# Optimization experiments

Hardware: AMD Instinct MI355X
Metric: run time of the kernel (lower is better)

The kernel has to match this reference:

```python
import jax, jax.numpy as jnp
import numpy as np
from jax import lax

# Covers the fully-specified prefix of ColorHead.downgrade (the high-headroom region):
# ColorDownsample(16) -> ModePool2d(11,1,1) -> Conv1x1(3->32) -> depthwise Conv1x1 -> BN -> LeakyReLU
#   -> Conv1x1(32->32) -> depthwise Conv1x1 -> BN -> LeakyReLU

NBINS = 17
KS = 11  # ModePool2d kernel_size
EPS = 1e-5
SLOPE = 0.01  # torch LeakyReLU default negative_slope


def color_downsample(x, down=16.0):
    return jnp.round(x * 255.0 / down) * down / 256.0


def mode_pool2d(x, kernel_size=KS, stride=1, padding=1):
    # Equivalent to torch unfold + scatter_add histogram + argmax, but computes
    # per-bin counts with a windowed sum over one-hot indicators (no giant unfold).
    xp = jnp.pad(x, ((0, 0), (0, 0), (padding, padding), (padding, padding)))
    bins = jnp.clip(jnp.round(xp * 16.0), 0.0, 16.0).astype(jnp.int32)  # [B,C,H,W]
    onehot = (bins[:, :, None, :, :] == jnp.arange(NBINS, dtype=jnp.int32)[None, None, :, None, None]).astype(x.dtype)  # [B,C,17,H,W]
    counts = lax.reduce_window(
        onehot, jnp.array(0, x.dtype), lax.add,
        window_dimensions=(1, 1, 1, kernel_size, kernel_size),
        window_strides=(1, 1, 1, stride, stride),
        padding='VALID')  # [B,C,17,Ho,Wo]
    mode_bins = jnp.argmax(counts, axis=2)  # first max, like torch argmax
    return mode_bins.astype(x.dtype) / 16.0


def conv1x1(x, w, b):
    # w: [O, C], b: [O]
    return jnp.einsum('bchw,oc->bohw', x, w) + b[None, :, None, None]


def dwconv1x1(x, w, b):
    # depthwise 1x1 (groups == channels): per-channel affine. w: [C], b: [C]
    return x * w[None, :, None, None] + b[None, :, None, None]


def batchnorm(x, gamma, beta):
    # training-mode BN: batch statistics over (B,H,W)
    mean = jnp.mean(x, axis=(0, 2, 3), keepdims=True)
    var = jnp.var(x, axis=(0, 2, 3), keepdims=True)
    xn = (x - mean) * lax.rsqrt(var + EPS)
    return xn * gamma[None, :, None, None] + beta[None, :, None, None]


def leaky_relu(x):
    return jnp.where(x >= 0, x, SLOPE * x)


def setup_inputs() -> dict:
    key = jax.random.key(0)
    ks = jax.random.split(key, 8)
    C_in, C_h = 3, 32
    x = jax.random.uniform(ks[0], (8, C_in, 512, 512), dtype=jnp.float32)
    w1 = jax.random.normal(ks[1], (C_h, C_in), dtype=jnp.float32) * 0.1
    b1 = jnp.zeros((C_h,), jnp.float32)
    wd1 = jax.random.normal(ks[2], (C_h,), dtype=jnp.float32) * 0.1 + 1.0
    bd1 = jnp.zeros((C_h,), jnp.float32)
    g1 = jnp.ones((C_h,), jnp.float32)
    be1 = jnp.zeros((C_h,), jnp.float32)
    w2 = jax.random.normal(ks[3], (C_h, C_h), dtype=jnp.float32) * 0.1
    b2 = jnp.zeros((C_h,), jnp.float32)
    wd2 = jax.random.normal(ks[4], (C_h,), dtype=jnp.float32) * 0.1 + 1.0
    bd2 = jnp.zeros((C_h,), jnp.float32)
    g2 = jnp.ones((C_h,), jnp.float32)
    be2 = jnp.zeros((C_h,), jnp.float32)
    return dict(x=x, w1=w1, b1=b1, wd1=wd1, bd1=bd1, g1=g1, be1=be1,
                w2=w2, b2=b2, wd2=wd2, bd2=bd2, g2=g2, be2=be2)


def reference(x, w1, b1, wd1, bd1, g1, be1, w2, b2, wd2, bd2, g2, be2):
    h = color_downsample(x)
    h = mode_pool2d(h)                      # [B,3,504,504]
    h = conv1x1(h, w1, b1)                  # [B,32,504,504]
    h = dwconv1x1(h, wd1, bd1)
    h = leaky_relu(batchnorm(h, g1, be1))
    h = conv1x1(h, w2, b2)
    h = dwconv1x1(h, wd2, bd2)
    h = leaky_relu(batchnorm(h, g2, be2))
    return h
```

## Files before the change

### kernel.cpp

```cpp
#include <hip/hip_runtime.h>
#include <hip/hip_bf16.h>

typedef unsigned char u8;
typedef unsigned short u16;
typedef unsigned int u32;

#define PP     254016
#define PADW   514
#define PADP   264196
#define NPIX   2032128
#define NTRIP  4913
#define N_F    2032128.0
#define RROWS  14

__device__ __forceinline__ float bf2f(__hip_bfloat16 h){ return __bfloat162float(h); }
__device__ __forceinline__ u32 f2bf(float f){
  u32 u = __float_as_uint(f);
  return ((u + 0x7FFFu + ((u >> 16) & 1u)) >> 16);
}
__device__ __forceinline__ float ldv(const void* p, int i, u32 f){
  return f ? ((const float*)p)[i] : bf2f(((const __hip_bfloat16*)p)[i]);
}

__global__ __launch_bounds__(256) void k_init(const u16* __restrict__ xw, u32* __restrict__ flag,
                                              u32* __restrict__ hist){
  int t = threadIdx.x;
  for (int i=t; i<NTRIP; i+=256) hist[i] = 0u;
  if (t < 64){
    u32 bad = 0;
    for (int i=t; i<1024; i+=64) bad |= (u32)(xw[i] >> 15);
    int anybad = __any((int)bad);
    if (t == 0) *flag = anybad ? 1u : 0u;
  }
}

__global__ __launch_bounds__(256) void k_bins(const void* __restrict__ x, u8* __restrict__ bins,
                                              const u32* __restrict__ flag){
  u32 f = *flag;
  int plane = blockIdx.y;
  int pix = blockIdx.x*256 + threadIdx.x;
  if (pix >= PADP) return;
  int r = pix / PADW; int c = pix - r*PADW;
  u8 v = 0;
  if (r >= 1 && r <= 512 && c >= 1 && c <= 512){
    float xv = ldv(x, plane*262144 + (r-1)*512 + (c-1), f);
    v = (u8)(int)rintf((xv * 255.0f) * 0.0625f);
  }
  bins[(size_t)plane*PADP + pix] = v;
}

__global__ __launch_bounds__(512) void k_mode(const u8* __restrict__ bins, u8* __restrict__ modes){
  int plane = blockIdx.y;
  int r0 = blockIdx.x * RROWS;
  const u8* bp = bins + (size_t)plane*PADP;
  u8* mp = modes + (size_t)plane*PP;
  __shared__ u32 A0[2][516], A1[2][516];
  int t = threadIdx.x;
  bool extra = (t < 2);
  u32 v0=0, v1=0, w0=0, w1=0;
  #pragma unroll 1
  for (int j=0; j<11; j++){
    int row = r0 + j;
    { int b = bp[row*PADW + t]; u32 d = 1u << ((b & 7)*4);
      v0 += (b < 8) ? d : 0u; v1 += (b >= 8 && b < 16) ? d : 0u; }
    if (extra){ int b = bp[row*PADW + 512 + t]; u32 d = 1u << ((b & 7)*4);
      w0 += (b < 8) ? d : 0u; w1 += (b >= 8 && b < 16) ? d : 0u; }
  }
  A0[0][t] = v0; A1[0][t] = v1;
  if (extra){ A0[0][512+t] = w0; A1[0][512+t] = w1; }
  __syncthreads();
  for (int i=0; i<RROWS; i++){
    int r = r0 + i;
    int cur = i & 1, nxt = cur ^ 1;
    if (t < 504){
      u32 h0=0,h1=0,h2=0,h3=0;
      #pragma unroll
      for (int dx=0; dx<11; dx++){
        u32 n0 = A0[cur][t+dx], n1 = A1[cur][t+dx];
        h0 += n0 & 0x0F0F0F0Fu;
        h1 += (n0 >> 4) & 0x0F0F0F0Fu;
        h2 += n1 & 0x0F0F0F0Fu;
        h3 += (n1 >> 4) & 0x0F0F0F0Fu;
      }
      u32 T = h0 + h1 + h2 + h3;
      u32 s = (T & 0xFFu) + ((T>>8)&0xFFu) + ((T>>16)&0xFFu) + (T>>24);
      u32 best = (121u - s) << 5;
      #pragma unroll
      for (int b=0;b<16;b++){
        u32 word = (b & 1) ? ((b < 8) ? h1 : h3) : ((b < 8) ? h0 : h2);
        u32 cnt = (word >> (((b >> 1) & 3) * 8)) & 0xFFu;
        u32 key = (cnt << 5) | (u32)(16 - b);
        best = (key > best) ? key : best;
      }
      mp[r*504 + t] = (u8)(16u - (best & 31u));
    }
    if (i+1 < RROWS){
      { int b = bp[r*PADW + t]; u32 d = 1u << ((b & 7)*4);
        v0 -= (b < 8) ? d : 0u; v1 -= (b >= 8 && b < 16) ? d : 0u; }
      { int b = bp[(r+11)*PADW + t]; u32 d = 1u << ((b & 7)*4);
        v0 += (b < 8) ? d : 0u; v1 += (b >= 8 && b < 16) ? d : 0u; }
      if (extra){
        { int b = bp[r*PADW + 512 + t]; u32 d = 1u << ((b & 7)*4);
          w0 -= (b < 8) ? d : 0u; w1 -= (b >= 8 && b < 16) ? d : 0u; }
        { int b = bp[(r+11)*PADW + 512 + t]; u32 d = 1u << ((b & 7)*4);
          w0 += (b < 8) ? d : 0u; w1 += (b >= 8 && b < 16) ? d : 0u; }
      }
      A0[nxt][t] = v0; A1[nxt][t] = v1;
      if (extra){ A0[nxt][512+t] = w0; A1[nxt][512+t] = w1; }
    }
    __syncthreads();
  }
}

__global__ __launch_bounds__(256) void k_triple(const u8* __restrict__ modes, u16* __restrict__ triple, u32* __restrict__ hist){
  __shared__ u32 lh[NTRIP];
  for (int i=threadIdx.x;i<NTRIP;i+=256) lh[i]=0;
  __syncthreads();
  int stride = gridDim.x*256;
  for (int p = blockIdx.x*256 + threadIdx.x; p < NPIX; p += stride){
    int bimg = p / PP; int pix = p - bimg*PP;
    const u8* mb = modes + (size_t)bimg*3*PP + pix;
    int m0 = mb[0], m1 = mb[PP], m2 = mb[2*PP];
    int idx = (m0*17 + m1)*17 + m2;
    triple[p] = (u16)idx;
    atomicAdd(&lh[idx], 1u);
  }
  __syncthreads();
  for (int i=threadIdx.x;i<NTRIP;i+=256){ u32 v = lh[i]; if (v) atomicAdd(&hist[i], v); }
}

__device__ __forceinline__ void compute_P1(const u32* __restrict__ hist,
    const void* w1, const void* b1, const void* wd1, const void* bd1,
    const void* g1, const void* be1, u32 f, float* sP ,
    u32* wred , u32* mom ){
  u32 a0=0,a1=0,a2=0,a3=0,a4=0,a5=0,a6=0,a7=0,a8=0;
  for (int t=threadIdx.x; t<NTRIP; t+=256){
    u32 c = hist[t];
    int m2 = t % 17; int tt = t/17; int m1 = tt % 17; int m0 = tt/17;
    a0 += c*m0; a1 += c*m1; a2 += c*m2;
    a3 += c*m0*m0; a4 += c*m1*m1; a5 += c*m2*m2;
    a6 += c*m0*m1; a7 += c*m0*m2; a8 += c*m1*m2;
  }
  #pragma unroll
  for (int s=1; s<64; s<<=1){
    a0 += __shfl_xor(a0,s); a1 += __shfl_xor(a1,s); a2 += __shfl_xor(a2,s);
    a3 += __shfl_xor(a3,s); a4 += __shfl_xor(a4,s); a5 += __shfl_xor(a5,s);
    a6 += __shfl_xor(a6,s); a7 += __shfl_xor(a7,s); a8 += __shfl_xor(a8,s);
  }
  int wv = threadIdx.x >> 6;
  if ((threadIdx.x & 63) == 0){
    wred[wv*9+0]=a0; wred[wv*9+1]=a1; wred[wv*9+2]=a2; wred[wv*9+3]=a3; wred[wv*9+4]=a4;
    wred[wv*9+5]=a5; wred[wv*9+6]=a6; wred[wv*9+7]=a7; wred[wv*9+8]=a8;
  }
  __syncthreads();
  if (threadIdx.x < 9) mom[threadIdx.x] = wred[threadIdx.x] + wred[9+threadIdx.x] + wred[18+threadIdx.x] + wred[27+threadIdx.x];
  __syncthreads();
  if (threadIdx.x < 32){
    int o = threadIdx.x;
    double wd = ldv(wd1,o,f);
    double q0 = wd*ldv(w1,o*3+0,f), q1 = wd*ldv(w1,o*3+1,f), q2 = wd*ldv(w1,o*3+2,f);
    double qc = wd*ldv(b1,o,f) + ldv(bd1,o,f);
    double S0=mom[0],S1=mom[1],S2=mom[2],S00=mom[3],S11=mom[4],S22=mom[5],S01=mom[6],S02=mom[7],S12=mom[8];
    double lin = (q0*S0 + q1*S1 + q2*S2) * (1.0/16.0);
    double mean = lin/N_F + qc;
    double quad = (q0*q0*S00 + q1*q1*S11 + q2*q2*S22 + 2.0*(q0*q1*S01 + q0*q2*S02 + q1*q2*S12)) * (1.0/256.0);
    double Ev2 = quad/N_F + 2.0*qc*lin/N_F + qc*qc;
    double var = Ev2 - mean*mean;
    double rstd = 1.0 / sqrt(var + 1e-5);
    double A = rstd * ldv(g1,o,f);
    double B = ldv(be1,o,f) - mean*A;
    sP[o]      = (float)(q0*A);
    sP[32+o]   = (float)(q1*A);
    sP[64+o]   = (float)(q2*A);
    sP[96+o]   = (float)(qc*A + B);
  }
  __syncthreads();
}

__global__ __launch_bounds__(256) void k_stats2(const u32* __restrict__ hist,
    const void* w1, const void* b1, const void* wd1, const void* bd1, const void* g1, const void* be1,
    const void* w2, const void* b2, const void* wd2, const void* bd2,
    double* __restrict__ sums2, const u32* __restrict__ flag){
  u32 f = *flag;
  int o = blockIdx.x;
  __shared__ float sP[128];
  __shared__ u32 wred[36], mom[9];
  __shared__ float sw[32];
  compute_P1(hist, w1,b1,wd1,bd1,g1,be1, f, sP, wred, mom);
  for (int i=threadIdx.x;i<32;i+=256) sw[i] = ldv(w2, o*32+i, f);
  __syncthreads();
  float wd = ldv(wd2, o, f);
  float cc = wd * ldv(b2, o, f) + ldv(bd2, o, f);
  double s=0.0, q=0.0;
  for (int t=threadIdx.x; t<NTRIP; t+=256){
    int m2 = t % 17; int tt = t / 17; int m1 = tt % 17; int m0 = tt / 17;
    float f0 = m0*(1.f/16.f), f1 = m1*(1.f/16.f), f2 = m2*(1.f/16.f);
    float dot = 0.f;
    #pragma unroll
    for (int c=0;c<32;c++){
      float u = sP[c]*f0 + sP[32+c]*f1 + sP[64+c]*f2 + sP[96+c];
      float y = (u >= 0.f) ? u : 0.01f*u;
      dot += sw[c]*y;
    }
    float v2 = wd*dot + cc;
    double cn = (double)hist[t];
    s += cn*(double)v2;
    q += cn*(double)v2*(double)v2;
  }
  __shared__ double red[256];
  red[threadIdx.x]=s; __syncthreads();
  for (int off=128; off>0; off>>=1){ if (threadIdx.x<off) red[threadIdx.x]+=red[threadIdx.x+off]; __syncthreads(); }
  if (threadIdx.x==0) sums2[o]=red[0];
  __syncthreads();
  red[threadIdx.x]=q; __syncthreads();
  for (int off=128; off>0; off>>=1){ if (threadIdx.x<off) red[threadIdx.x]+=red[threadIdx.x+off]; __syncthreads(); }
  if (threadIdx.x==0) sums2[32+o]=red[0];
}

__global__ __launch_bounds__(256) void k_lut(const u32* __restrict__ hist, const double* __restrict__ sums2,
    const void* w1, const void* b1, const void* wd1, const void* bd1, const void* g1, const void* be1,
    const void* w2, const void* b2, const void* wd2, const void* bd2,
    const void* g2, const void* be2,
    float* __restrict__ lutf, u32* __restrict__ lutb, const u32* __restrict__ flag){
  u32 f = *flag;
  __shared__ float sP[128];
  __shared__ u32 wred[36], mom[9];
  __shared__ float sw[1024];
  __shared__ float ka[32], kb[32];
  compute_P1(hist, w1,b1,wd1,bd1,g1,be1, f, sP, wred, mom);
  for (int i=threadIdx.x;i<1024;i+=256) sw[i]=ldv(w2, i, f);
  if (threadIdx.x < 32){
    int o = threadIdx.x;
    double mean = sums2[o] / N_F;
    double var  = sums2[32+o] / N_F - mean*mean;
    double rstd = 1.0 / sqrt(var + 1e-5);
    double A = rstd * (double)ldv(g2, o, f);
    double B = (double)ldv(be2, o, f) - mean*A;
    double wd = (double)ldv(wd2, o, f);
    ka[o] = (float)(wd*A);
    kb[o] = (float)((wd*(double)ldv(b2, o, f) + (double)ldv(bd2, o, f))*A + B);
  }
  __syncthreads();
  int t = blockIdx.x*256 + threadIdx.x;
  if (t >= NTRIP) return;
  int m2 = t % 17; int tt = t/17; int m1 = tt % 17; int m0 = tt/17;
  float f0=m0*(1.f/16.f), f1=m1*(1.f/16.f), f2=m2*(1.f/16.f);
  float y1[32];
  #pragma unroll
  for (int c=0;c<32;c++){
    float u = sP[c]*f0 + sP[32+c]*f1 + sP[64+c]*f2 + sP[96+c];
    y1[c] = (u>=0.f)?u:0.01f*u;
  }
  float y2[32];
  #pragma unroll
  for (int o=0;o<32;o++){
    float dot=0.f;
    #pragma unroll
    for (int c=0;c<32;c++) dot += sw[o*32+c]*y1[c];
    float v = dot*ka[o] + kb[o];
    y2[o] = (v>=0.f)?v:0.01f*v;
    lutf[t*32+o] = y2[o];
  }
  #pragma unroll
  for (int j=0;j<16;j++)
    lutb[t*16+j] = f2bf(y2[2*j]) | (f2bf(y2[2*j+1]) << 16);
}

__global__ __launch_bounds__(256) void k_out(const u16* __restrict__ triple, const float* __restrict__ lutf,
                                             const u32* __restrict__ lutb,
                                             void* __restrict__ out, const u32* __restrict__ flag){
  u32 f = *flag;
  int g = blockIdx.x*256 + threadIdx.x;
  if (g >= NPIX/2) return;
  int p0 = g*2;
  int bimg = p0 / PP; int pix = p0 - bimg*PP;
  u32 tt = *(const u32*)(triple + p0);
  u32 ia = tt & 0xFFFFu, ib = tt >> 16;
  if (f){
    const float4* La = (const float4*)(lutf + (size_t)ia*32);
    const float4* Lb = (const float4*)(lutf + (size_t)ib*32);
    float* ob = (float*)out + (size_t)bimg*32*PP + pix;
    #pragma unroll
    for (int j=0;j<8;j++){
      float4 a = La[j]; float4 b = Lb[j];
      float2 v;
      v.x=a.x; v.y=b.x; *(float2*)(ob + (size_t)(4*j+0)*PP) = v;
      v.x=a.y; v.y=b.y; *(float2*)(ob + (size_t)(4*j+1)*PP) = v;
      v.x=a.z; v.y=b.z; *(float2*)(ob + (size_t)(4*j+2)*PP) = v;
      v.x=a.w; v.y=b.w; *(float2*)(ob + (size_t)(4*j+3)*PP) = v;
    }
  } else {
    const uint4* La = (const uint4*)(lutb + (size_t)ia*16);
    const uint4* Lb = (const uint4*)(lutb + (size_t)ib*16);
    u16* ob = (u16*)out + (size_t)bimg*32*PP + pix;
    #pragma unroll
    for (int j=0;j<4;j++){
      uint4 A = La[j]; uint4 B = Lb[j];
      *(u32*)(ob + (size_t)(8*j+0)*PP) = __builtin_amdgcn_perm(B.x, A.x, 0x05040100u);
      *(u32*)(ob + (size_t)(8*j+1)*PP) = __builtin_amdgcn_perm(B.x, A.x, 0x07060302u);
      *(u32*)(ob + (size_t)(8*j+2)*PP) = __builtin_amdgcn_perm(B.y, A.y, 0x05040100u);
      *(u32*)(ob + (size_t)(8*j+3)*PP) = __builtin_amdgcn_perm(B.y, A.y, 0x07060302u);
      *(u32*)(ob + (size_t)(8*j+4)*PP) = __builtin_amdgcn_perm(B.z, A.z, 0x05040100u);
      *(u32*)(ob + (size_t)(8*j+5)*PP) = __builtin_amdgcn_perm(B.z, A.z, 0x07060302u);
      *(u32*)(ob + (size_t)(8*j+6)*PP) = __builtin_amdgcn_perm(B.w, A.w, 0x05040100u);
      *(u32*)(ob + (size_t)(8*j+7)*PP) = __builtin_amdgcn_perm(B.w, A.w, 0x07060302u);
    }
  }
}

extern "C" void kernel_launch(void* const* d_in, const int* in_sizes, int n_in,
                              void* d_out, int out_size, void* d_ws, size_t ws_size,
                              hipStream_t stream){
  const void* x   = d_in[0];
  const void* w1  = d_in[1];
  const void* b1  = d_in[2];
  const void* wd1 = d_in[3];
  const void* bd1 = d_in[4];
  const void* g1  = d_in[5];
  const void* be1 = d_in[6];
  const void* w2  = d_in[7];
  const void* b2  = d_in[8];
  const void* wd2 = d_in[9];
  const void* bd2 = d_in[10];
  const void* g2  = d_in[11];
  const void* be2 = d_in[12];

  char* w = (char*)d_ws;
  auto alloc = [&](size_t bytes)->char* { char* p = w; w += (bytes + 255) & ~(size_t)255; return p; };
  u32*   flag   = (u32*)  alloc(256);
  u8*    bins   = (u8*)   alloc(24ull*PADP);
  u8*    modes  = (u8*)   alloc(24ull*PP);
  u16*   triple = (u16*)  alloc(2ull*NPIX);
  u32*   hist   = (u32*)  alloc(4ull*NTRIP);
  double* sums2 = (double*)alloc(64ull*8);
  float* lutf   = (float*)alloc(4ull*NTRIP*32);
  u32*   lutb   = (u32*)  alloc(4ull*NTRIP*16);

  k_init<<<dim3(1), 256, 0, stream>>>((const u16*)x, flag, hist);
  k_bins<<<dim3((PADP+255)/256, 24), 256, 0, stream>>>(x, bins, flag);
  k_mode<<<dim3(36, 24), 512, 0, stream>>>(bins, modes);
  k_triple<<<dim3(1984), 256, 0, stream>>>(modes, triple, hist);
  k_stats2<<<dim3(32), 256, 0, stream>>>(hist, w1,b1,wd1,bd1,g1,be1, w2,b2,wd2,bd2, sums2, flag);
  k_lut<<<dim3((NTRIP+255)/256), 256, 0, stream>>>(hist, sums2, w1,b1,wd1,bd1,g1,be1,
                                                   w2,b2,wd2,bd2, g2,be2, lutf, lutb, flag);
  k_out<<<dim3((NPIX/2)/256), 256, 0, stream>>>(triple, lutf, lutb, d_out, flag);
}
```

Measured before the change: 442.6 us.

## Fuse binning, mode pooling and triple histogram into one kernel

Replaces the separate bin, mode-pool and triple/histogram kernels with a single kernel that reads the input directly, keeps all three channels' sliding column counts in 64-bit packed registers, and emits the triple index plus a shared-memory histogram. The intermediate bins and modes buffers and their global round trips go away, and the argmax uses packed 16-bit max operations. In exchange it reloads an input row for each slide step, uses a shorter row strip per block (4 rows, so more redundant 11-row warmup reads), and puts more shared-memory atomics in each block.

```diff
diff --git a/kernel.cpp b/kernel.cpp
--- a/kernel.cpp
+++ b/kernel.cpp
@@ -4,14 +4,14 @@
 typedef unsigned char u8;
 typedef unsigned short u16;
 typedef unsigned int u32;
+typedef unsigned long long u64;
 
 #define PP     254016
-#define PADW   514
-#define PADP   264196
 #define NPIX   2032128
 #define NTRIP  4913
 #define N_F    2032128.0
-#define RROWS  14
+#define RROWS  4
+#define NRB    126
 
 __device__ __forceinline__ float bf2f(__hip_bfloat16 h){ return __bfloat162float(h); }
 __device__ __forceinline__ u32 f2bf(float f){
@@ -21,6 +21,23 @@
 __device__ __forceinline__ float ldv(const void* p, int i, u32 f){
   return f ? ((const float*)p)[i] : bf2f(((const __hip_bfloat16*)p)[i]);
 }
+
+typedef unsigned short us2 __attribute__((ext_vector_type(2)));
+__device__ __forceinline__ u32 pkmax(u32 a, u32 b){
+  us2 x = __builtin_bit_cast(us2, a);
+  us2 y = __builtin_bit_cast(us2, b);
+  us2 r = __builtin_elementwise_max(x, y);
+  return __builtin_bit_cast(u32, r);
+}
+
+__device__ __forceinline__ u32 getbin(const void* x, u32 f, int img, int ch, int pr, int pc){
+  if ((u32)(pr-1) < 512u && (u32)(pc-1) < 512u){
+    float xv = ldv(x, ((img*3+ch)*512 + (pr-1))*512 + (pc-1), f);
+    return (u32)(int)rintf(xv * 255.0f * 0.0625f);
+  }
+  return 0u;
+}
+__device__ __forceinline__ u64 bdelta(u32 b){ return (b < 16u) ? (1ull << (b*4)) : 0ull; }
 
 __global__ __launch_bounds__(256) void k_init(const u16* __restrict__ xw, u32* __restrict__ flag,
                                               u32* __restrict__ hist){
@@ -34,99 +51,116 @@
   }
 }
 
-__global__ __launch_bounds__(256) void k_bins(const void* __restrict__ x, u8* __restrict__ bins,
-                                              const u32* __restrict__ flag){
+__global__ __launch_bounds__(512) void k_fused(const void* __restrict__ x, const u32* __restrict__ flag,
+                                               u16* __restrict__ triple, u32* __restrict__ hist){
   u32 f = *flag;
-  int plane = blockIdx.y;
-  int pix = blockIdx.x*256 + threadIdx.x;
-  if (pix >= PADP) return;
-  int r = pix / PADW; int c = pix - r*PADW;
-  u8 v = 0;
-  if (r >= 1 && r <= 512 && c >= 1 && c <= 512){
-    float xv = ldv(x, plane*262144 + (r-1)*512 + (c-1), f);
-    v = (u8)(int)rintf((xv * 255.0f) * 0.0625f);
-  }
-  bins[(size_t)plane*PADP + pix] = v;
-}
-
-__global__ __launch_bounds__(512) void k_mode(const u8* __restrict__ bins, u8* __restrict__ modes){
-  int plane = blockIdx.y;
+  int img = blockIdx.y;
   int r0 = blockIdx.x * RROWS;
-  const u8* bp = bins + (size_t)plane*PADP;
-  u8* mp = modes + (size_t)plane*PP;
-  __shared__ u32 A0[2][516], A1[2][516];
   int t = threadIdx.x;
+  __shared__ u64 CNT[3][518];
+  __shared__ u32 lh[NTRIP];
+  for (int i=t; i<NTRIP; i+=512) lh[i] = 0u;
+
   bool extra = (t < 2);
-  u32 v0=0, v1=0, w0=0, w1=0;
-  #pragma unroll 1
+  int colB = 512 + t;
+  u64 v[3] = {0,0,0}, vb[3] = {0,0,0};
+  u64 rn[3] = {0,0,0}, rnb[3] = {0,0,0};
+  u32 r16[3] = {0,0,0}, r16b[3] = {0,0,0};
+
   for (int j=0; j<11; j++){
-    int row = r0 + j;
-    { int b = bp[row*PADW + t]; u32 d = 1u << ((b & 7)*4);
-      v0 += (b < 8) ? d : 0u; v1 += (b >= 8 && b < 16) ? d : 0u; }
-    if (extra){ int b = bp[row*PADW + 512 + t]; u32 d = 1u << ((b & 7)*4);
-      w0 += (b < 8) ? d : 0u; w1 += (b >= 8 && b < 16) ? d : 0u; }
-  }
-  A0[0][t] = v0; A1[0][t] = v1;
-  if (extra){ A0[0][512+t] = w0; A1[0][512+t] = w1; }
-  __syncthreads();
+    int pr = r0 + j;
+    #pragma unroll
+    for (int ch=0; ch<3; ch++){
+      u32 b = getbin(x, f, img, ch, pr, t);
+      v[ch] += bdelta(b);
+      rn[ch] = (rn[ch] << 4) | (u64)(b & 15u);
+      r16[ch] = (r16[ch] << 1) | (b >> 4);
+    }
+    if (extra){
+      #pragma unroll
+      for (int ch=0; ch<3; ch++){
+        u32 b = getbin(x, f, img, ch, pr, colB);
+        vb[ch] += bdelta(b);
+        rnb[ch] = (rnb[ch] << 4) | (u64)(b & 15u);
+        r16b[ch] = (r16b[ch] << 1) | (b >> 4);
+      }
+    }
+  }
+  #pragma unroll
+  for (int ch=0; ch<3; ch++) CNT[ch][t] = v[ch];
+  if (extra){
+    #pragma unroll
+    for (int ch=0; ch<3; ch++) CNT[ch][colB] = vb[ch];
+  }
+  __syncthreads();
+
   for (int i=0; i<RROWS; i++){
     int r = r0 + i;
-    int cur = i & 1, nxt = cur ^ 1;
     if (t < 504){
-      u32 h0=0,h1=0,h2=0,h3=0;
+      u32 m3[3];
       #pragma unroll
-      for (int dx=0; dx<11; dx++){
-        u32 n0 = A0[cur][t+dx], n1 = A1[cur][t+dx];
-        h0 += n0 & 0x0F0F0F0Fu;
-        h1 += (n0 >> 4) & 0x0F0F0F0Fu;
-        h2 += n1 & 0x0F0F0F0Fu;
-        h3 += (n1 >> 4) & 0x0F0F0F0Fu;
+      for (int ch=0; ch<3; ch++){
+        u64 he = 0, ho = 0;
+        #pragma unroll
+        for (int dx=0; dx<11; dx++){
+          u64 n = CNT[ch][t+dx];
+          he += n & 0x0F0F0F0F0F0F0F0Full;
+          ho += (n >> 4) & 0x0F0F0F0F0F0F0F0Full;
+        }
+        u64 T = he + ho;
+        u32 T2 = (u32)T + (u32)(T >> 32);
+        u32 s = (T2 & 0xFFu) + ((T2>>8)&0xFFu) + ((T2>>16)&0xFFu) + (T2>>24);
+        u32 e_lo = (u32)he, e_hi = (u32)(he >> 32);
+        u32 o_lo = (u32)ho, o_hi = (u32)(ho >> 32);
+        u32 k0 = ((e_lo & 0x00FF00FFu) << 5) | 0x000C0010u;
+        u32 k1 = ((e_lo >> 3) & 0x1FE01FE0u) | 0x000A000Eu;
+        u32 k2 = ((e_hi & 0x00FF00FFu) << 5) | 0x00040008u;
+        u32 k3 = ((e_hi >> 3) & 0x1FE01FE0u) | 0x00020006u;
+        u32 k4 = ((o_lo & 0x00FF00FFu) << 5) | 0x000B000Fu;
+        u32 k5 = ((o_lo >> 3) & 0x1FE01FE0u) | 0x0009000Du;
+        u32 k6 = ((o_hi & 0x00FF00FFu) << 5) | 0x00030007u;
+        u32 k7 = ((o_hi >> 3) & 0x1FE01FE0u) | 0x00010005u;
+        u32 m = pkmax(pkmax(pkmax(k0,k1), pkmax(k2,k3)), pkmax(pkmax(k4,k5), pkmax(k6,k7)));
+        u32 best = m >> 16, blo = m & 0xFFFFu;
+        best = best > blo ? best : blo;
+        u32 k16 = (121u - s) << 5;
+        best = best > k16 ? best : k16;
+        m3[ch] = 16u - (best & 31u);
       }
-      u32 T = h0 + h1 + h2 + h3;
-      u32 s = (T & 0xFFu) + ((T>>8)&0xFFu) + ((T>>16)&0xFFu) + (T>>24);
-      u32 best = (121u - s) << 5;
+      u32 idx = (m3[0]*17u + m3[1])*17u + m3[2];
+      triple[img*PP + r*504 + t] = (u16)idx;
+      atomicAdd(&lh[idx], 1u);
+    }
+    __syncthreads();
+    if (i+1 < RROWS){
       #pragma unroll
-      for (int b=0;b<16;b++){
-        u32 word = (b & 1) ? ((b < 8) ? h1 : h3) : ((b < 8) ? h0 : h2);
-        u32 cnt = (word >> (((b >> 1) & 3) * 8)) & 0xFFu;
-        u32 key = (cnt << 5) | (u32)(16 - b);
-        best = (key > best) ? key : best;
+      for (int ch=0; ch<3; ch++){
+        u32 nb = getbin(x, f, img, ch, r+11, t);
+        rn[ch] = (rn[ch] << 4) | (u64)(nb & 15u);
+        r16[ch] = (r16[ch] << 1) | (nb >> 4);
+        u32 ob = (u32)((rn[ch] >> 44) & 15u);
+        u32 o16 = (r16[ch] >> 11) & 1u;
+        v[ch] += bdelta(nb);
+        v[ch] -= o16 ? 0ull : (1ull << (ob*4));
+        CNT[ch][t] = v[ch];
       }
-      mp[r*504 + t] = (u8)(16u - (best & 31u));
-    }
-    if (i+1 < RROWS){
-      { int b = bp[r*PADW + t]; u32 d = 1u << ((b & 7)*4);
-        v0 -= (b < 8) ? d : 0u; v1 -= (b >= 8 && b < 16) ? d : 0u; }
-      { int b = bp[(r+11)*PADW + t]; u32 d = 1u << ((b & 7)*4);
-        v0 += (b < 8) ? d : 0u; v1 += (b >= 8 && b < 16) ? d : 0u; }
       if (extra){
-        { int b = bp[r*PADW + 512 + t]; u32 d = 1u << ((b & 7)*4);
-          w0 -= (b < 8) ? d : 0u; w1 -= (b >= 8 && b < 16) ? d : 0u; }
-        { int b = bp[(r+11)*PADW + 512 + t]; u32 d = 1u << ((b & 7)*4);
-          w0 += (b < 8) ? d : 0u; w1 += (b >= 8 && b < 16) ? d : 0u; }
+        #pragma unroll
+        for (int ch=0; ch<3; ch++){
+          u32 nb = getbin(x, f, img, ch, r+11, colB);
+          rnb[ch] = (rnb[ch] << 4) | (u64)(nb & 15u);
+          r16b[ch] = (r16b[ch] << 1) | (nb >> 4);
+          u32 ob = (u32)((rnb[ch] >> 44) & 15u);
+          u32 o16 = (r16b[ch] >> 11) & 1u;
+          vb[ch] += bdelta(nb);
+          vb[ch] -= o16 ? 0ull : (1ull << (ob*4));
+          CNT[ch][colB] = vb[ch];
+        }
       }
-      A0[nxt][t] = v0; A1[nxt][t] = v1;
-      if (extra){ A0[nxt][512+t] = w0; A1[nxt][512+t] = w1; }
     }
     __syncthreads();
   }
-}
-
-__global__ __launch_bounds__(256) void k_triple(const u8* __restrict__ modes, u16* __restrict__ triple, u32* __restrict__ hist){
-  __shared__ u32 lh[NTRIP];
-  for (int i=threadIdx.x;i<NTRIP;i+=256) lh[i]=0;
-  __syncthreads();
-  int stride = gridDim.x*256;
-  for (int p = blockIdx.x*256 + threadIdx.x; p < NPIX; p += stride){
-    int bimg = p / PP; int pix = p - bimg*PP;
-    const u8* mb = modes + (size_t)bimg*3*PP + pix;
-    int m0 = mb[0], m1 = mb[PP], m2 = mb[2*PP];
-    int idx = (m0*17 + m1)*17 + m2;
-    triple[p] = (u16)idx;
-    atomicAdd(&lh[idx], 1u);
-  }
-  __syncthreads();
-  for (int i=threadIdx.x;i<NTRIP;i+=256){ u32 v = lh[i]; if (v) atomicAdd(&hist[i], v); }
+  for (int i=t; i<NTRIP; i+=512){ u32 c = lh[i]; if (c) atomicAdd(&hist[i], c); }
 }
 
 __device__ __forceinline__ void compute_P1(const u32* __restrict__ hist,
@@ -328,8 +362,6 @@
   char* w = (char*)d_ws;
   auto alloc = [&](size_t bytes)->char* { char* p = w; w += (bytes + 255) & ~(size_t)255; return p; };
   u32*   flag   = (u32*)  alloc(256);
-  u8*    bins   = (u8*)   alloc(24ull*PADP);
-  u8*    modes  = (u8*)   alloc(24ull*PP);
   u16*   triple = (u16*)  alloc(2ull*NPIX);
   u32*   hist   = (u32*)  alloc(4ull*NTRIP);
   double* sums2 = (double*)alloc(64ull*8);
@@ -337,9 +369,7 @@
   u32*   lutb   = (u32*)  alloc(4ull*NTRIP*16);
 
   k_init<<<dim3(1), 256, 0, stream>>>((const u16*)x, flag, hist);
-  k_bins<<<dim3((PADP+255)/256, 24), 256, 0, stream>>>(x, bins, flag);
-  k_mode<<<dim3(36, 24), 512, 0, stream>>>(bins, modes);
-  k_triple<<<dim3(1984), 256, 0, stream>>>(modes, triple, hist);
+  k_fused<<<dim3(NRB, 8), 512, 0, stream>>>(x, flag, triple, hist);
   k_stats2<<<dim3(32), 256, 0, stream>>>(hist, w1,b1,wd1,bd1,g1,be1, w2,b2,wd2,bd2, sums2, flag);
   k_lut<<<dim3((NTRIP+255)/256), 256, 0, stream>>>(hist, sums2, w1,b1,wd1,bd1,g1,be1,
                                                    w2,b2,wd2,bd2, g2,be2, lutf, lutb, flag);
```

Measured after the change: 387.4 us. 1.14x faster.
